# Performance work log

Measured on AMD Instinct MI355X. Metric: run time of the kernel, lower is better.

## Reference

```python
import jax, jax.numpy as jnp
import numpy as np

N, E, H, NF, EF = 50000, 400000, 128, 10, 10


def setup_inputs() -> dict:
    key = jax.random.key(0)
    ks = iter(jax.random.split(key, 24))
    rn = lambda shape, s=0.1: jax.random.normal(next(ks), shape, jnp.float32) * s
    z = lambda shape: jnp.zeros(shape, jnp.float32)
    o = lambda shape: jnp.ones(shape, jnp.float32)
    return {
        "x": jax.random.normal(next(ks), (N, NF), jnp.float32),
        "edge_index": jax.random.randint(next(ks), (2, E), 0, N, jnp.int32),
        "edge_attr": jax.random.normal(next(ks), (E, EF), jnp.float32),
        "ne_w": rn((NF, H)), "ne_b": z(H), "ne_g": o(H), "ne_beta": z(H),
        "ee_w": rn((EF, H)), "ee_b": z(H), "ee_g": o(H), "ee_beta": z(H),
        "gate_w": rn((3 * H, H)), "gate_b": z(H),
        "gatA_w": rn((2, H, H)), "gatA_asrc": rn((2, 8, 16)), "gatA_adst": rn((2, 8, 16)), "gatA_bias": z((2, H)),
        "gatB_w": rn((H, H)), "gatB_asrc": rn((1, H)), "gatB_adst": rn((1, H)), "gatB_bias": z(H),
        "ln_g": o((3, H)), "ln_b": z((3, H)),
        "c1_w": rn((2 * H, H)), "c1_b": z(H), "cl1_g": o(H), "cl1_b": z(H),
        "c2_w": rn((H, H // 2)), "c2_b": z(H // 2), "cl2_g": o(H // 2), "cl2_b": z(H // 2),
        "c3_w": rn((H // 2, 2)), "c3_b": z(2),
    }


def _ln(x, g, b):
    m = x.mean(-1, keepdims=True)
    v = ((x - m) ** 2).mean(-1, keepdims=True)
    return (x - m) / jnp.sqrt(v + 1e-5) * g + b


def _gat(h, src, dst, n, w, asrc, adst, bias, concat):
    # PyG GATConv: lin (no bias), per-edge leaky_relu score, segment softmax over dst, scatter-add
    heads, dout = asrc.shape
    xp = (h @ w).reshape(n, heads, dout)             # [N, heads, dout]
    a_s = (xp * asrc).sum(-1)                        # [N, heads]
    a_d = (xp * adst).sum(-1)
    e = jax.nn.leaky_relu(a_s[src] + a_d[dst], 0.2)  # [E2, heads]
    m = jax.ops.segment_max(e, dst, num_segments=n)
    ex = jnp.exp(e - m[dst])
    s = jax.ops.segment_sum(ex, dst, num_segments=n)
    alpha = ex / s[dst]                               # [E2, heads]
    out = jax.ops.segment_sum(xp[src] * alpha[..., None], dst, num_segments=n)  # [N, heads, dout]
    out = out.reshape(n, heads * dout) if concat else out.mean(1)
    return out + bias


def reference(x, edge_index, edge_attr, ne_w, ne_b, ne_g, ne_beta, ee_w, ee_b, ee_g, ee_beta,
              gate_w, gate_b, gatA_w, gatA_asrc, gatA_adst, gatA_bias, gatB_w, gatB_asrc,
              gatB_adst, gatB_bias, ln_g, ln_b, c1_w, c1_b, cl1_g, cl1_b, c2_w, c2_b,
              cl2_g, cl2_b, c3_w, c3_b):
    n = x.shape[0]
    row, col = edge_index[0], edge_index[1]
    loops = jnp.arange(n, dtype=edge_index.dtype)     # GATConv add_self_loops=True
    src_sl = jnp.concatenate([row, loops])
    dst_sl = jnp.concatenate([col, loops])

    h = jax.nn.relu(_ln(x @ ne_w + ne_b, ne_g, ne_beta))      # node encoder (dropout=eval)
    for l in range(2):
        h = _gat(h, src_sl, dst_sl, n, gatA_w[l], gatA_asrc[l], gatA_adst[l], gatA_bias[l], True)
        h = jax.nn.relu(_ln(h, ln_g[l], ln_b[l]))
    h = _gat(h, src_sl, dst_sl, n, gatB_w, gatB_asrc, gatB_adst, gatB_bias, False)
    h = jax.nn.relu(_ln(h, ln_g[2], ln_b[2]))

    s = h[row]
    d = h[col]
    e = jax.nn.relu(_ln(edge_attr @ ee_w + ee_b, ee_g, ee_beta))  # edge encoder
    gate = jax.nn.sigmoid(jnp.concatenate([s, d, e], axis=1) @ gate_w + gate_b)
    s = s + gate * e
    d = d + gate * e

    zc = jax.nn.relu(_ln(jnp.concatenate([s, d], axis=1) @ c1_w + c1_b, cl1_g, cl1_b))
    zc = jax.nn.relu(_ln(zc @ c2_w + c2_b, cl2_g, cl2_b))
    return zc @ c3_w + c3_b                                   # [E, num_classes]
```

## Files before the change

kernel.cpp:

```cpp
#include <hip/hip_runtime.h>
#include <hip/hip_bf16.h>

#define H 128
#define NFEAT 10
#define EFEAT 10
#define XPS 144

typedef __attribute__((ext_vector_type(8))) short bf16x8;
typedef __attribute__((ext_vector_type(4))) float f32x4;
typedef __attribute__((ext_vector_type(16))) float f32x16;
typedef __attribute__((ext_vector_type(4))) unsigned u32x4;
typedef __attribute__((ext_vector_type(2))) unsigned u32x2;

__device__ __forceinline__ float bflo(unsigned v) { return __uint_as_float(v << 16); }
__device__ __forceinline__ float bfhi(unsigned v) { return __uint_as_float(v & 0xffff0000u); }
__device__ __forceinline__ unsigned bfpack(float a, float b) {
    __hip_bfloat16 h0 = __float2bfloat16(a), h1 = __float2bfloat16(b);
    return (unsigned)(*(unsigned short*)&h0) | ((unsigned)(*(unsigned short*)&h1) << 16);
}
__device__ __forceinline__ bf16x8 cast8(u32x4 v) { return __builtin_bit_cast(bf16x8, v); }

__device__ __forceinline__ bf16x8 frag_from_pack(const unsigned* w, int b2) {
    u32x4 t;
    t.x = w[b2 * 4 + 0];
    t.y = w[b2 * 4 + 1];
    t.z = w[b2 * 4 + 2];
    t.w = w[b2 * 4 + 3];
    return cast8(t);
}

template<int NT>
__device__ __forceinline__ void bias_ln_relu_pack(f32x16* acc, const float* __restrict__ bias,
        const float* __restrict__ g, const float* __restrict__ beta,
        int hh, float invn, unsigned (*pk)[8]) {
    float sm = 0.f;
#pragma unroll
    for (int m = 0; m < NT; m++) {
#pragma unroll
        for (int P = 0; P < 4; P++) {
            f32x4 bv = *(const f32x4*)&bias[m * 32 + P * 8 + hh * 4];
#pragma unroll
            for (int u = 0; u < 4; u++) {
                float v = acc[m][P * 4 + u] + bv[u];
                acc[m][P * 4 + u] = v;
                sm += v;
            }
        }
    }
    sm += __shfl_xor(sm, 32, 64);
    float mean = sm * invn;
    float q = 0.f;
#pragma unroll
    for (int m = 0; m < NT; m++) {
#pragma unroll
        for (int r = 0; r < 16; r++) { float d = acc[m][r] - mean; q += d * d; }
    }
    q += __shfl_xor(q, 32, 64);
    float rstd = rsqrtf(q * invn + 1e-5f);
#pragma unroll
    for (int m = 0; m < NT; m++) {
#pragma unroll
        for (int P = 0; P < 4; P++) {
            f32x4 gv = *(const f32x4*)&g[m * 32 + P * 8 + hh * 4];
            f32x4 bz = *(const f32x4*)&beta[m * 32 + P * 8 + hh * 4];
#pragma unroll
            for (int u = 0; u < 4; u++) {
                float y = fmaxf((acc[m][P * 4 + u] - mean) * rstd * gv[u] + bz[u], 0.f);
                acc[m][P * 4 + u] = y;
            }
        }
    }
#pragma unroll
    for (int m = 0; m < NT; m++) {
#pragma unroll
        for (int p = 0; p < 8; p++) pk[m][p] = bfpack(acc[m][2 * p], acc[m][2 * p + 1]);
    }
}

__global__ __launch_bounds__(256) void k_degree(const int* __restrict__ col,
                                                int* __restrict__ deg, int E, int N) {
    int i = blockIdx.x * blockDim.x + threadIdx.x;
    int E2 = E + N;
    if (i < E2) {
        int d = (i < E) ? col[i] : (i - E);
        atomicAdd(&deg[d], 1);
    }
}

__global__ __launch_bounds__(1024) void k_scan(const int* __restrict__ deg,
                                               int* __restrict__ offs,
                                               int* __restrict__ cursor, int N) {
    __shared__ int ps[1024];
    int t = threadIdx.x;
    int chunk = (N + 1023) / 1024;
    int begin = t * chunk;
    int end = begin + chunk; if (end > N) end = N;
    int s = 0;
    for (int i = begin; i < end; i++) s += deg[i];
    if (begin >= N) s = 0;
    ps[t] = s;
    __syncthreads();
    for (int off = 1; off < 1024; off <<= 1) {
        int v = (t >= off) ? ps[t - off] : 0;
        __syncthreads();
        ps[t] += v;
        __syncthreads();
    }
    int run = (t == 0) ? 0 : ps[t - 1];
    if (begin < N) {
        for (int i = begin; i < end; i++) {
            offs[i] = run;
            cursor[i] = run;
            run += deg[i];
        }
    }
    if (t == 1023) offs[N] = ps[1023];
}

__global__ __launch_bounds__(256) void k_scatter(const int* __restrict__ rowp,
                                                 const int* __restrict__ colp,
                                                 int* __restrict__ cursor,
                                                 int* __restrict__ srcs, int E, int N) {
    int i = blockIdx.x * blockDim.x + threadIdx.x;
    if (i < E + N) {
        int s, d;
        if (i < E) { s = rowp[i]; d = colp[i]; }
        else       { s = i - E;  d = i - E; }
        int pos = atomicAdd(&cursor[d], 1);
        srcs[pos] = s;
    }
}

__global__ __launch_bounds__(256) void k_node_enc(const float* __restrict__ x,
                                                  const float* __restrict__ wm,
                                                  const float* __restrict__ b,
                                                  const float* __restrict__ g,
                                                  const float* __restrict__ beta,
                                                  __hip_bfloat16* __restrict__ h, int N) {
    int t = threadIdx.x;
    int w = t >> 6, l = t & 63;
    int n = blockIdx.x * 4 + w;
    if (n >= N) return;
    float xs[NFEAT];
#pragma unroll
    for (int k = 0; k < NFEAT; k++) xs[k] = x[(size_t)n * NFEAT + k];
    float a0 = b[2 * l], a1 = b[2 * l + 1];
#pragma unroll
    for (int k = 0; k < NFEAT; k++) {
        float2 wv = *(const float2*)&wm[k * H + 2 * l];
        a0 += xs[k] * wv.x;
        a1 += xs[k] * wv.y;
    }
    float p = a0 + a1;
#pragma unroll
    for (int s = 1; s < 64; s <<= 1) p += __shfl_xor(p, s, 64);
    float mean = p * (1.0f / H);
    float d0 = a0 - mean, d1 = a1 - mean;
    float q = d0 * d0 + d1 * d1;
#pragma unroll
    for (int s = 1; s < 64; s <<= 1) q += __shfl_xor(q, s, 64);
    float rstd = rsqrtf(q * (1.0f / H) + 1e-5f);
    float y0 = fmaxf(d0 * rstd * g[2 * l] + beta[2 * l], 0.0f);
    float y1 = fmaxf(d1 * rstd * g[2 * l + 1] + beta[2 * l + 1], 0.0f);
    *(unsigned*)&h[(size_t)n * H + 2 * l] = bfpack(y0, y1);
}

__global__ __launch_bounds__(256, 2) void k_gat_xp_mfma(
        const __hip_bfloat16* __restrict__ h_bf,
        const __hip_bfloat16* __restrict__ wT,
        const float* __restrict__ asrc,
        const float* __restrict__ adst,
        __hip_bfloat16* __restrict__ xp_bf,
        float* __restrict__ a_d,
        int heads, int N) {
    __shared__ __hip_bfloat16 Ws[128 * 136];
    __shared__ __hip_bfloat16 As[64 * 136];
    int t = threadIdx.x;
    int n0 = blockIdx.x * 64;

#pragma unroll
    for (int it = 0; it < 2; it++) {
        int idx = it * 256 + t;
        int row = idx >> 2, seg = idx & 3;
        const uint4* src = (const uint4*)(wT + row * 128 + seg * 32);
        uint4 v0 = src[0], v1 = src[1], v2 = src[2], v3 = src[3];
        uint4* dst = (uint4*)&Ws[row * 136 + seg * 32];
        dst[0] = v0; dst[1] = v1; dst[2] = v2; dst[3] = v3;
    }
    {
        int row = t >> 2, seg = t & 3;
        int n = n0 + row; if (n >= N) n = N - 1;
        const uint4* src = (const uint4*)(h_bf + (size_t)n * 128 + seg * 32);
        uint4 v0 = src[0], v1 = src[1], v2 = src[2], v3 = src[3];
        uint4* dst = (uint4*)&As[row * 136 + seg * 32];
        dst[0] = v0; dst[1] = v1; dst[2] = v2; dst[3] = v3;
    }
    __syncthreads();

    int w = t >> 6, l = t & 63, ln15 = l & 15, quad = l >> 4, q8 = quad * 8;
    f32x4 acc[8] = {};
#pragma unroll
    for (int k = 0; k < 128; k += 32) {
        bf16x8 af = *(const bf16x8*)&As[(w * 16 + ln15) * 136 + k + q8];
#pragma unroll
        for (int i = 0; i < 8; i++) {
            bf16x8 bfr = *(const bf16x8*)&Ws[(i * 16 + ln15) * 136 + k + q8];
            acc[i] = __builtin_amdgcn_mfma_f32_16x16x32_bf16(af, bfr, acc[i], 0, 0, 0);
        }
    }

    if (heads == 8) {
#pragma unroll
        for (int i = 0; i < 8; i++) {
            float av = asrc[i * 16 + ln15], dvv = adst[i * 16 + ln15];
            float ps[4], pd[4];
#pragma unroll
            for (int r = 0; r < 4; r++) { ps[r] = acc[i][r] * av; pd[r] = acc[i][r] * dvv; }
#pragma unroll
            for (int s = 1; s < 16; s <<= 1) {
#pragma unroll
                for (int r = 0; r < 4; r++) {
                    ps[r] += __shfl_xor(ps[r], s, 64);
                    pd[r] += __shfl_xor(pd[r], s, 64);
                }
            }
            if (ln15 == 0) {
#pragma unroll
                for (int r = 0; r < 4; r++) {
                    int n = n0 + w * 16 + quad * 4 + r;
                    if (n < N) {
                        *(float*)&xp_bf[(size_t)n * XPS + 128 + 2 * i] = ps[r];
                        a_d[(size_t)n * 8 + i] = pd[r];
                    }
                }
            }
        }
    } else {
        float ps[4] = {0, 0, 0, 0}, pd[4] = {0, 0, 0, 0};
#pragma unroll
        for (int i = 0; i < 8; i++) {
            float av = asrc[i * 16 + ln15], dvv = adst[i * 16 + ln15];
#pragma unroll
            for (int r = 0; r < 4; r++) { ps[r] += acc[i][r] * av; pd[r] += acc[i][r] * dvv; }
        }
#pragma unroll
        for (int s = 1; s < 16; s <<= 1) {
#pragma unroll
            for (int r = 0; r < 4; r++) {
                ps[r] += __shfl_xor(ps[r], s, 64);
                pd[r] += __shfl_xor(pd[r], s, 64);
            }
        }
        if (ln15 == 0) {
#pragma unroll
            for (int r = 0; r < 4; r++) {
                int n = n0 + w * 16 + quad * 4 + r;
                if (n < N) {
                    *(float*)&xp_bf[(size_t)n * XPS + 128] = ps[r];
                    a_d[n] = pd[r];
                }
            }
        }
    }

#pragma unroll
    for (int i = 0; i < 8; i++) {
#pragma unroll
        for (int r = 0; r < 4; r++) {
            int n = n0 + w * 16 + quad * 4 + r;
            if (n < N) xp_bf[(size_t)n * XPS + i * 16 + ln15] = __float2bfloat16(acc[i][r]);
        }
    }
}

__global__ __launch_bounds__(256) void k_gat_agg(const __hip_bfloat16* __restrict__ xp,
                                                 const float* __restrict__ a_d,
                                                 const int* __restrict__ offs,
                                                 const int* __restrict__ srcs,
                                                 const float* __restrict__ bias,
                                                 const float* __restrict__ g,
                                                 const float* __restrict__ b,
                                                 __hip_bfloat16* __restrict__ hout,
                                                 int heads, int N) {
    int t = threadIdx.x;
    int w = t >> 6, l = t & 63;
    int n = blockIdx.x * 4 + w;
    if (n >= N) return;
    int head = (heads == 8) ? (l >> 3) : 0;
    float adv = a_d[(size_t)n * heads + head];
    int s0 = offs[n], s1 = offs[n + 1];
    float acc0 = 0.0f, acc1 = 0.0f, den = 0.0f;
    int j = s0;
    for (; j + 4 <= s1; j += 4) {
        int s_[4];
#pragma unroll
        for (int u = 0; u < 4; u++) s_[u] = srcs[j + u];
        float e_[4]; unsigned v_[4];
#pragma unroll
        for (int u = 0; u < 4; u++) {
            const __hip_bfloat16* xr = xp + (size_t)s_[u] * XPS;
            e_[u] = ((const float*)xr)[64 + head];
            v_[u] = *(const unsigned*)&xr[2 * l];
        }
#pragma unroll
        for (int u = 0; u < 4; u++) {
            float e = e_[u] + adv;
            e = (e >= 0.0f) ? e : 0.2f * e;
            float ex = __expf(e);
            den += ex;
            acc0 += ex * bflo(v_[u]);
            acc1 += ex * bfhi(v_[u]);
        }
    }
    for (; j < s1; j++) {
        int s = srcs[j];
        const __hip_bfloat16* xr = xp + (size_t)s * XPS;
        float e = ((const float*)xr)[64 + head] + adv;
        e = (e >= 0.0f) ? e : 0.2f * e;
        float ex = __expf(e);
        den += ex;
        unsigned v = *(const unsigned*)&xr[2 * l];
        acc0 += ex * bflo(v);
        acc1 += ex * bfhi(v);
    }
    float inv = 1.0f / den;
    float v0 = acc0 * inv + bias[2 * l];
    float v1 = acc1 * inv + bias[2 * l + 1];
    float p = v0 + v1;
#pragma unroll
    for (int s = 1; s < 64; s <<= 1) p += __shfl_xor(p, s, 64);
    float mean = p * (1.0f / H);
    float d0 = v0 - mean, d1 = v1 - mean;
    float q = d0 * d0 + d1 * d1;
#pragma unroll
    for (int s = 1; s < 64; s <<= 1) q += __shfl_xor(q, s, 64);
    float rstd = rsqrtf(q * (1.0f / H) + 1e-5f);
    float y0 = fmaxf(d0 * rstd * g[2 * l] + b[2 * l], 0.0f);
    float y1 = fmaxf(d1 * rstd * g[2 * l + 1] + b[2 * l + 1], 0.0f);
    *(unsigned*)&hout[(size_t)n * H + 2 * l] = bfpack(y0, y1);
}

__global__ __launch_bounds__(256) void k_wprep(const float* __restrict__ gate_w,
                                               const float* __restrict__ c1_w,
                                               const float* __restrict__ c2_w,
                                               const float* __restrict__ gatA_w,
                                               const float* __restrict__ gatB_w,
                                               const float* __restrict__ ee_w,
                                               __hip_bfloat16* __restrict__ gate_sw,
                                               __hip_bfloat16* __restrict__ c1_sw,
                                               __hip_bfloat16* __restrict__ c2_sw,
                                               __hip_bfloat16* __restrict__ wT3,
                                               __hip_bfloat16* __restrict__ ee_sw) {
    int i = blockIdx.x * blockDim.x + threadIdx.x;
    if (i < 49152) {
        int j = i & 7, l = (i >> 3) & 63, s = i >> 9;
        int m = s & 3, ks = s >> 2;
        int hh = l >> 5;
        int k;
        if (ks < 8) k = 256 + ks * 16 + 4 * hh + (j & 3) + 8 * (j >> 2);
        else        k = (ks - 8) * 16 + hh * 8 + j;
        int n = m * 32 + (l & 31);
        gate_sw[i] = __float2bfloat16(gate_w[k * 128 + n]);
    } else if (i < 81920) {
        int mm = i - 49152;
        int j = mm & 7, l = (mm >> 3) & 63, s = mm >> 9;
        int m = s & 3, ks = s >> 2;
        int k = ks * 16 + 4 * (l >> 5) + (j & 3) + 8 * (j >> 2);
        int n = m * 32 + (l & 31);
        c1_sw[mm] = __float2bfloat16(c1_w[k * 128 + n]);
    } else if (i < 90112) {
        int mm = i - 81920;
        int j = mm & 7, l = (mm >> 3) & 63, s = mm >> 9;
        int m = s & 1, ks = s >> 1;
        int k = ks * 16 + 4 * (l >> 5) + (j & 3) + 8 * (j >> 2);
        int n = m * 32 + (l & 31);
        c2_sw[mm] = __float2bfloat16(c2_w[k * 64 + n]);
    } else if (i < 139264) {
        int m = i - 90112;
        int mat = m / 16384, r = m % 16384;
        int n = r / 128, k = r % 128;
        const float* src = (mat < 2) ? (gatA_w + (size_t)mat * 16384) : gatB_w;
        wT3[m] = __float2bfloat16(src[k * 128 + n]);
    } else if (i < 141312) {
        int mm = i - 139264;
        int j = mm & 7, l = (mm >> 3) & 63, s = mm >> 9;
        int k = (l >> 5) * 8 + j;
        int n = s * 32 + (l & 31);
        ee_sw[mm] = (k < EFEAT) ? __float2bfloat16(ee_w[k * 128 + n]) : __float2bfloat16(0.0f);
    }
}

__global__ __launch_bounds__(256, 2) void k_edge_cls_mfma32(
        const __hip_bfloat16* __restrict__ h_bf,
        const int* __restrict__ rowp, const int* __restrict__ colp,
        const float* __restrict__ eattr,
        const __hip_bfloat16* __restrict__ ee_fa, const float* __restrict__ ee_b,
        const float* __restrict__ ee_g, const float* __restrict__ ee_beta,
        const __hip_bfloat16* __restrict__ gate_fa, const float* __restrict__ gate_b,
        const __hip_bfloat16* __restrict__ c1_fa, const float* __restrict__ c1_b,
        const float* __restrict__ cl1_g, const float* __restrict__ cl1_b,
        const __hip_bfloat16* __restrict__ c2_fa, const float* __restrict__ c2_b,
        const float* __restrict__ cl2_g, const float* __restrict__ cl2_b,
        const float* __restrict__ c3_w, const float* __restrict__ c3_b,
        float* __restrict__ out, int E) {
    int t = threadIdx.x;
    int w = t >> 6, l = t & 63;
    int hh = l >> 5, e32 = l & 31;
    int eIdx = blockIdx.x * 128 + w * 32 + e32;
    int eF = (eIdx < E) ? eIdx : (E - 1);
    int ri = rowp[eF], ci = colp[eF];
    const unsigned short* rS = (const unsigned short*)h_bf + (size_t)ri * H;
    const unsigned short* rD = (const unsigned short*)h_bf + (size_t)ci * H;

    unsigned efw[4][8];
    {
        const char* eb = (const char*)(eattr + (size_t)eF * EFEAT);
        float2 p0 = *(const float2*)(eb + (hh << 5));
        float2 p1 = *(const float2*)(eb + 8);
        float2 p2 = *(const float2*)(eb + 16);
        float2 p3 = *(const float2*)(eb + 24);
        if (hh) { p1.x = p1.y = 0.f; p2.x = p2.y = 0.f; p3.x = p3.y = 0.f; }
        u32x4 bwv;
        bwv.x = bfpack(p0.x, p0.y);
        bwv.y = bfpack(p1.x, p1.y);
        bwv.z = bfpack(p2.x, p2.y);
        bwv.w = bfpack(p3.x, p3.y);
        bf16x8 bb = cast8(bwv);
        f32x16 acc[4] = {};
#pragma unroll
        for (int m = 0; m < 4; m++) {
            bf16x8 a = *(const bf16x8*)(ee_fa + ((size_t)m * 64 + l) * 8);
            acc[m] = __builtin_amdgcn_mfma_f32_32x32x16_bf16(a, bb, acc[m], 0, 0, 0);
        }
        bias_ln_relu_pack<4>(acc, ee_b, ee_g, ee_beta, hh, 1.f / 128.f, efw);
    }

    f32x16 acc1[4] = {};
    {
        bf16x8 af[4];
#pragma unroll
        for (int s = 0; s < 4; s++) af[s] = *(const bf16x8*)(gate_fa + ((size_t)s * 64 + l) * 8);
#pragma unroll
        for (int ks = 0; ks < 8; ks++) {
            int m = ks >> 1, b2 = ks & 1;
            bf16x8 bb = frag_from_pack(efw[m], b2);
#pragma unroll
            for (int mt = 0; mt < 4; mt++) {
                int s = ks * 4 + mt;
                bf16x8 a = af[s & 3];
                af[s & 3] = *(const bf16x8*)(gate_fa + ((size_t)(s + 4) * 64 + l) * 8);
                acc1[mt] = __builtin_amdgcn_mfma_f32_32x32x16_bf16(a, bb, acc1[mt], 0, 0, 0);
            }
        }
#pragma unroll
        for (int ks = 8; ks < 24; ks++) {
            const unsigned short* rp = (ks < 16) ? rS : rD;
            int kl = ((ks - 8) & 7) * 16 + hh * 8;
            bf16x8 bb = *(const bf16x8*)(rp + kl);
#pragma unroll
            for (int mt = 0; mt < 4; mt++) {
                int s = ks * 4 + mt;
                bf16x8 a = af[s & 3];
                if (s + 4 < 96) af[s & 3] = *(const bf16x8*)(gate_fa + ((size_t)(s + 4) * 64 + l) * 8);
                acc1[mt] = __builtin_amdgcn_mfma_f32_32x32x16_bf16(a, bb, acc1[mt], 0, 0, 0);
            }
        }
    }

    unsigned sw[4][8], dw[4][8];
    {
#pragma unroll
        for (int m = 0; m < 4; m++) {
#pragma unroll
            for (int P = 0; P < 4; P++) {
                int f0 = m * 32 + P * 8 + hh * 4;
                f32x4 gb = *(const f32x4*)&gate_b[f0];
                u32x2 sv = *(const u32x2*)(rS + f0);
                u32x2 dv = *(const u32x2*)(rD + f0);
#pragma unroll
                for (int u2 = 0; u2 < 2; u2++) {
                    int p = P * 2 + u2;
                    unsigned svw = u2 ? sv.y : sv.x;
                    unsigned dvw = u2 ? dv.y : dv.x;
                    float g0 = acc1[m][2 * p] + gb[2 * u2];
                    float g1 = acc1[m][2 * p + 1] + gb[2 * u2 + 1];
                    g0 = 1.f / (1.f + __expf(-g0));
                    g1 = 1.f / (1.f + __expf(-g1));
                    float e0 = bflo(efw[m][p]), e1 = bfhi(efw[m][p]);
                    sw[m][p] = bfpack(bflo(svw) + g0 * e0, bfhi(svw) + g1 * e1);
                    dw[m][p] = bfpack(bflo(dvw) + g0 * e0, bfhi(dvw) + g1 * e1);
                }
            }
        }
    }

    unsigned z1w[4][8];
    {
        f32x16 acc2[4] = {};
        bf16x8 af[4];
#pragma unroll
        for (int s = 0; s < 4; s++) af[s] = *(const bf16x8*)(c1_fa + ((size_t)s * 64 + l) * 8);
#pragma unroll
        for (int ks = 0; ks < 8; ks++) {
            int m = ks >> 1, b2 = ks & 1;
            bf16x8 bb = frag_from_pack(sw[m], b2);
#pragma unroll
            for (int mt = 0; mt < 4; mt++) {
                int s = ks * 4 + mt;
                bf16x8 a = af[s & 3];
                af[s & 3] = *(const bf16x8*)(c1_fa + ((size_t)(s + 4) * 64 + l) * 8);
                acc2[mt] = __builtin_amdgcn_mfma_f32_32x32x16_bf16(a, bb, acc2[mt], 0, 0, 0);
            }
        }
#pragma unroll
        for (int ks = 8; ks < 16; ks++) {
            int kk = ks - 8;
            int m = kk >> 1, b2 = kk & 1;
            bf16x8 bb = frag_from_pack(dw[m], b2);
#pragma unroll
            for (int mt = 0; mt < 4; mt++) {
                int s = ks * 4 + mt;
                bf16x8 a = af[s & 3];
                if (s + 4 < 64) af[s & 3] = *(const bf16x8*)(c1_fa + ((size_t)(s + 4) * 64 + l) * 8);
                acc2[mt] = __builtin_amdgcn_mfma_f32_32x32x16_bf16(a, bb, acc2[mt], 0, 0, 0);
            }
        }
        bias_ln_relu_pack<4>(acc2, c1_b, cl1_g, cl1_b, hh, 1.f / 128.f, z1w);
    }

    {
        f32x16 acc3[2] = {};
        bf16x8 af[4];
#pragma unroll
        for (int s = 0; s < 4; s++) af[s] = *(const bf16x8*)(c2_fa + ((size_t)s * 64 + l) * 8);
#pragma unroll
        for (int ks = 0; ks < 8; ks++) {
            int m = ks >> 1, b2 = ks & 1;
            bf16x8 bb = frag_from_pack(z1w[m], b2);
#pragma unroll
            for (int mt = 0; mt < 2; mt++) {
                int s = ks * 2 + mt;
                bf16x8 a = af[s & 3];
                if (s + 4 < 16) af[s & 3] = *(const bf16x8*)(c2_fa + ((size_t)(s + 4) * 64 + l) * 8);
                acc3[mt] = __builtin_amdgcn_mfma_f32_32x32x16_bf16(a, bb, acc3[mt], 0, 0, 0);
            }
        }
        float sm = 0.f;
#pragma unroll
        for (int m = 0; m < 2; m++) {
#pragma unroll
            for (int P = 0; P < 4; P++) {
                f32x4 bv = *(const f32x4*)&c2_b[m * 32 + P * 8 + hh * 4];
#pragma unroll
                for (int u = 0; u < 4; u++) {
                    float v = acc3[m][P * 4 + u] + bv[u];
                    acc3[m][P * 4 + u] = v;
                    sm += v;
                }
            }
        }
        sm += __shfl_xor(sm, 32, 64);
        float mean = sm * (1.f / 64.f);
        float q = 0.f;
#pragma unroll
        for (int m = 0; m < 2; m++) {
#pragma unroll
            for (int r = 0; r < 16; r++) { float d = acc3[m][r] - mean; q += d * d; }
        }
        q += __shfl_xor(q, 32, 64);
        float rstd = rsqrtf(q * (1.f / 64.f) + 1e-5f);
        float s0 = 0.f, s1 = 0.f;
#pragma unroll
        for (int m = 0; m < 2; m++) {
#pragma unroll
            for (int P = 0; P < 4; P++) {
                int f0 = m * 32 + P * 8 + hh * 4;
                f32x4 gv = *(const f32x4*)&cl2_g[f0];
                f32x4 bz = *(const f32x4*)&cl2_b[f0];
                f32x4 wA = *(const f32x4*)&c3_w[f0 * 2];
                f32x4 wB = *(const f32x4*)&c3_w[f0 * 2 + 4];
#pragma unroll
                for (int u = 0; u < 4; u++) {
                    float y = fmaxf((acc3[m][P * 4 + u] - mean) * rstd * gv[u] + bz[u], 0.f);
                    float wc0 = (u < 2) ? wA[2 * u] : wB[2 * u - 4];
                    float wc1 = (u < 2) ? wA[2 * u + 1] : wB[2 * u - 3];
                    s0 += y * wc0;
                    s1 += y * wc1;
                }
            }
        }
        s0 += __shfl_xor(s0, 32, 64);
        s1 += __shfl_xor(s1, 32, 64);
        if (hh == 0 && eIdx < E) {
            float2 o; o.x = s0 + c3_b[0]; o.y = s1 + c3_b[1];
            *(float2*)&out[(size_t)eIdx * 2] = o;
        }
    }
}

extern "C" void kernel_launch(void* const* d_in, const int* in_sizes, int n_in,
                              void* d_out, int out_size, void* d_ws, size_t ws_size,
                              hipStream_t stream) {
    const float* x        = (const float*)d_in[0];
    const int*   eidx     = (const int*)d_in[1];
    const float* eattr    = (const float*)d_in[2];
    const float* ne_w     = (const float*)d_in[3];
    const float* ne_b     = (const float*)d_in[4];
    const float* ne_g     = (const float*)d_in[5];
    const float* ne_beta  = (const float*)d_in[6];
    const float* ee_w     = (const float*)d_in[7];
    const float* ee_b     = (const float*)d_in[8];
    const float* ee_g     = (const float*)d_in[9];
    const float* ee_beta  = (const float*)d_in[10];
    const float* gate_w   = (const float*)d_in[11];
    const float* gate_b   = (const float*)d_in[12];
    const float* gatA_w   = (const float*)d_in[13];
    const float* gatA_as  = (const float*)d_in[14];
    const float* gatA_ad  = (const float*)d_in[15];
    const float* gatA_bias= (const float*)d_in[16];
    const float* gatB_w   = (const float*)d_in[17];
    const float* gatB_as  = (const float*)d_in[18];
    const float* gatB_ad  = (const float*)d_in[19];
    const float* gatB_bias= (const float*)d_in[20];
    const float* ln_g     = (const float*)d_in[21];
    const float* ln_b     = (const float*)d_in[22];
    const float* c1_w     = (const float*)d_in[23];
    const float* c1_b     = (const float*)d_in[24];
    const float* cl1_g    = (const float*)d_in[25];
    const float* cl1_b    = (const float*)d_in[26];
    const float* c2_w     = (const float*)d_in[27];
    const float* c2_b     = (const float*)d_in[28];
    const float* cl2_g    = (const float*)d_in[29];
    const float* cl2_b    = (const float*)d_in[30];
    const float* c3_w     = (const float*)d_in[31];
    const float* c3_b     = (const float*)d_in[32];

    const int N = in_sizes[0] / NFEAT;
    const int E = in_sizes[1] / 2;
    const int E2 = E + N;
    const int* rowp = eidx;
    const int* colp = eidx + E;

    char* ws = (char*)d_ws;
    size_t off = 0;
    auto alloc = [&](size_t bytes) -> void* {
        void* p = ws + off;
        off = (off + bytes + 255) & ~(size_t)255;
        return p;
    };
    int*   deg    = (int*)alloc((size_t)N * 4);
    int*   cursor = (int*)alloc((size_t)N * 4);
    int*   offs   = (int*)alloc((size_t)(N + 1) * 4);
    int*   srcs   = (int*)alloc((size_t)E2 * 4);
    float* a_d    = (float*)alloc((size_t)N * 8 * 4);
    __hip_bfloat16* h_bfA  = (__hip_bfloat16*)alloc((size_t)N * H * 2);
    __hip_bfloat16* h_bfB  = (__hip_bfloat16*)alloc((size_t)N * H * 2);
    __hip_bfloat16* xp_bf  = (__hip_bfloat16*)alloc((size_t)N * XPS * 2);
    __hip_bfloat16* gate_sw= (__hip_bfloat16*)alloc((size_t)49152 * 2);
    __hip_bfloat16* c1_sw  = (__hip_bfloat16*)alloc((size_t)32768 * 2);
    __hip_bfloat16* c2_sw  = (__hip_bfloat16*)alloc((size_t)8192 * 2);
    __hip_bfloat16* wT3    = (__hip_bfloat16*)alloc((size_t)3 * 128 * 128 * 2);
    __hip_bfloat16* ee_sw  = (__hip_bfloat16*)alloc((size_t)4096 * 2);
    (void)ws_size;

    k_wprep<<<(141312 + 255) / 256, 256, 0, stream>>>(gate_w, c1_w, c2_w, gatA_w, gatB_w, ee_w,
                                                      gate_sw, c1_sw, c2_sw, wT3, ee_sw);

    hipMemsetAsync(deg, 0, (size_t)N * 4, stream);
    k_degree<<<(E2 + 255) / 256, 256, 0, stream>>>(colp, deg, E, N);
    k_scan<<<1, 1024, 0, stream>>>(deg, offs, cursor, N);
    k_scatter<<<(E2 + 255) / 256, 256, 0, stream>>>(rowp, colp, cursor, srcs, E, N);

    int ngrid = (N + 3) / 4;
    k_node_enc<<<ngrid, 256, 0, stream>>>(x, ne_w, ne_b, ne_g, ne_beta, h_bfA, N);

    int xpgrid = (N + 63) / 64;
    __hip_bfloat16* hin = h_bfA;
    __hip_bfloat16* hout = h_bfB;
    for (int l = 0; l < 2; l++) {
        k_gat_xp_mfma<<<xpgrid, 256, 0, stream>>>(hin, wT3 + (size_t)l * 16384,
                                                  gatA_as + l * H, gatA_ad + l * H,
                                                  xp_bf, a_d, 8, N);
        k_gat_agg<<<ngrid, 256, 0, stream>>>(xp_bf, a_d, offs, srcs,
                                             gatA_bias + l * H, ln_g + l * H, ln_b + l * H,
                                             hout, 8, N);
        __hip_bfloat16* tmp = hin; hin = hout; hout = tmp;
    }
    k_gat_xp_mfma<<<xpgrid, 256, 0, stream>>>(hin, wT3 + (size_t)2 * 16384,
                                              gatB_as, gatB_ad,
                                              xp_bf, a_d, 1, N);
    k_gat_agg<<<ngrid, 256, 0, stream>>>(xp_bf, a_d, offs, srcs,
                                         gatB_bias, ln_g + 2 * H, ln_b + 2 * H,
                                         hout, 1, N);

    k_edge_cls_mfma32<<<(E + 127) / 128, 256, 0, stream>>>(
        hout, rowp, colp, eattr,
        ee_sw, ee_b, ee_g, ee_beta,
        gate_sw, gate_b,
        c1_sw, c1_b, cl1_g, cl1_b,
        c2_sw, c2_b, cl2_g, cl2_b,
        c3_w, c3_b,
        (float*)d_out, E);
}
```

Before: 675.5 us.

## Precompute per-node gate and classifier projections, gather them per edge

Exploits linearity: the gate and first classifier layers applied to h[row] and h[col] are computed once per node (N×4 GEMMs into an fp32 table) instead of once per edge. The edge kernel then gathers these projections and only multiplies the gated edge-encoder term, using c1 weights summed over the src and dst halves. This cuts per-edge MFMA work from 24+16 K-steps to 8+8. In exchange it adds a 100MB fp32 table whose random gathers of 2KB rows per edge may become memory-bound.

After: 718.4 us. 6.4% more time.

```diff
diff --git a/kernel.cpp b/kernel.cpp
--- a/kernel.cpp
+++ b/kernel.cpp
@@ -346,58 +346,116 @@
                                                const float* __restrict__ gatA_w,
                                                const float* __restrict__ gatB_w,
                                                const float* __restrict__ ee_w,
-                                               __hip_bfloat16* __restrict__ gate_sw,
-                                               __hip_bfloat16* __restrict__ c1_sw,
+                                               __hip_bfloat16* __restrict__ gef_sw,
+                                               __hip_bfloat16* __restrict__ c1s_sw,
                                                __hip_bfloat16* __restrict__ c2_sw,
+                                               __hip_bfloat16* __restrict__ ee_sw,
                                                __hip_bfloat16* __restrict__ wT3,
-                                               __hip_bfloat16* __restrict__ ee_sw) {
+                                               __hip_bfloat16* __restrict__ wpre4) {
     int i = blockIdx.x * blockDim.x + threadIdx.x;
-    if (i < 49152) {
+    if (i < 16384) {
         int j = i & 7, l = (i >> 3) & 63, s = i >> 9;
         int m = s & 3, ks = s >> 2;
-        int hh = l >> 5;
-        int k;
-        if (ks < 8) k = 256 + ks * 16 + 4 * hh + (j & 3) + 8 * (j >> 2);
-        else        k = (ks - 8) * 16 + hh * 8 + j;
+        int k = 256 + ks * 16 + 4 * (l >> 5) + (j & 3) + 8 * (j >> 2);
         int n = m * 32 + (l & 31);
-        gate_sw[i] = __float2bfloat16(gate_w[k * 128 + n]);
-    } else if (i < 81920) {
-        int mm = i - 49152;
+        gef_sw[i] = __float2bfloat16(gate_w[k * 128 + n]);
+    } else if (i < 32768) {
+        int mm = i - 16384;
         int j = mm & 7, l = (mm >> 3) & 63, s = mm >> 9;
         int m = s & 3, ks = s >> 2;
         int k = ks * 16 + 4 * (l >> 5) + (j & 3) + 8 * (j >> 2);
         int n = m * 32 + (l & 31);
-        c1_sw[mm] = __float2bfloat16(c1_w[k * 128 + n]);
-    } else if (i < 90112) {
-        int mm = i - 81920;
+        c1s_sw[mm] = __float2bfloat16(c1_w[k * 128 + n] + c1_w[(128 + k) * 128 + n]);
+    } else if (i < 40960) {
+        int mm = i - 32768;
         int j = mm & 7, l = (mm >> 3) & 63, s = mm >> 9;
         int m = s & 1, ks = s >> 1;
         int k = ks * 16 + 4 * (l >> 5) + (j & 3) + 8 * (j >> 2);
         int n = m * 32 + (l & 31);
         c2_sw[mm] = __float2bfloat16(c2_w[k * 64 + n]);
-    } else if (i < 139264) {
-        int m = i - 90112;
-        int mat = m / 16384, r = m % 16384;
-        int n = r / 128, k = r % 128;
-        const float* src = (mat < 2) ? (gatA_w + (size_t)mat * 16384) : gatB_w;
-        wT3[m] = __float2bfloat16(src[k * 128 + n]);
-    } else if (i < 141312) {
-        int mm = i - 139264;
+    } else if (i < 43008) {
+        int mm = i - 40960;
         int j = mm & 7, l = (mm >> 3) & 63, s = mm >> 9;
         int k = (l >> 5) * 8 + j;
         int n = s * 32 + (l & 31);
         ee_sw[mm] = (k < EFEAT) ? __float2bfloat16(ee_w[k * 128 + n]) : __float2bfloat16(0.0f);
-    }
-}
-
-__global__ __launch_bounds__(256, 2) void k_edge_cls_mfma32(
+    } else if (i < 92160) {
+        int mm = i - 43008;
+        int mat = mm / 16384, r = mm % 16384;
+        int n = r / 128, k = r % 128;
+        const float* src = (mat < 2) ? (gatA_w + (size_t)mat * 16384) : gatB_w;
+        wT3[mm] = __float2bfloat16(src[k * 128 + n]);
+    } else if (i < 157696) {
+        int mm = i - 92160;
+        int mat = mm / 16384, r = mm % 16384;
+        int n = r / 128, k = r % 128;
+        float v = (mat == 0) ? gate_w[k * 128 + n]
+                : (mat == 1) ? gate_w[(128 + k) * 128 + n]
+                : (mat == 2) ? c1_w[k * 128 + n]
+                             : c1_w[(128 + k) * 128 + n];
+        wpre4[mm] = __float2bfloat16(v);
+    }
+}
+
+__global__ __launch_bounds__(256, 2) void k_pre_gemm(
         const __hip_bfloat16* __restrict__ h_bf,
+        const __hip_bfloat16* __restrict__ wpre4,
+        float* __restrict__ pre, int N) {
+    __shared__ __hip_bfloat16 Ws[128 * 136];
+    __shared__ __hip_bfloat16 As[64 * 136];
+    int t = threadIdx.x;
+    int n0 = blockIdx.x * 64;
+    int mat = blockIdx.y;
+    const __hip_bfloat16* wT = wpre4 + (size_t)mat * 16384;
+
+#pragma unroll
+    for (int it = 0; it < 2; it++) {
+        int idx = it * 256 + t;
+        int row = idx >> 2, seg = idx & 3;
+        const uint4* src = (const uint4*)(wT + row * 128 + seg * 32);
+        uint4 v0 = src[0], v1 = src[1], v2 = src[2], v3 = src[3];
+        uint4* dst = (uint4*)&Ws[row * 136 + seg * 32];
+        dst[0] = v0; dst[1] = v1; dst[2] = v2; dst[3] = v3;
+    }
+    {
+        int row = t >> 2, seg = t & 3;
+        int n = n0 + row; if (n >= N) n = N - 1;
+        const uint4* src = (const uint4*)(h_bf + (size_t)n * 128 + seg * 32);
+        uint4 v0 = src[0], v1 = src[1], v2 = src[2], v3 = src[3];
+        uint4* dst = (uint4*)&As[row * 136 + seg * 32];
+        dst[0] = v0; dst[1] = v1; dst[2] = v2; dst[3] = v3;
+    }
+    __syncthreads();
+
+    int w = t >> 6, l = t & 63, ln15 = l & 15, quad = l >> 4, q8 = quad * 8;
+    f32x4 acc[8] = {};
+#pragma unroll
+    for (int k = 0; k < 128; k += 32) {
+        bf16x8 af = *(const bf16x8*)&As[(w * 16 + ln15) * 136 + k + q8];
+#pragma unroll
+        for (int i = 0; i < 8; i++) {
+            bf16x8 bfr = *(const bf16x8*)&Ws[(i * 16 + ln15) * 136 + k + q8];
+            acc[i] = __builtin_amdgcn_mfma_f32_16x16x32_bf16(af, bfr, acc[i], 0, 0, 0);
+        }
+    }
+#pragma unroll
+    for (int i = 0; i < 8; i++) {
+#pragma unroll
+        for (int r = 0; r < 4; r++) {
+            int n = n0 + w * 16 + quad * 4 + r;
+            if (n < N) pre[(size_t)n * 512 + mat * 128 + i * 16 + ln15] = acc[i][r];
+        }
+    }
+}
+
+__global__ __launch_bounds__(256, 3) void k_edge_cls_v5(
         const int* __restrict__ rowp, const int* __restrict__ colp,
         const float* __restrict__ eattr,
+        const float* __restrict__ pre,
         const __hip_bfloat16* __restrict__ ee_fa, const float* __restrict__ ee_b,
         const float* __restrict__ ee_g, const float* __restrict__ ee_beta,
-        const __hip_bfloat16* __restrict__ gate_fa, const float* __restrict__ gate_b,
-        const __hip_bfloat16* __restrict__ c1_fa, const float* __restrict__ c1_b,
+        const __hip_bfloat16* __restrict__ gef_fa, const float* __restrict__ gate_b,
+        const __hip_bfloat16* __restrict__ c1s_fa, const float* __restrict__ c1_b,
         const float* __restrict__ cl1_g, const float* __restrict__ cl1_b,
         const __hip_bfloat16* __restrict__ c2_fa, const float* __restrict__ c2_b,
         const float* __restrict__ cl2_g, const float* __restrict__ cl2_b,
@@ -408,9 +466,8 @@
     int hh = l >> 5, e32 = l & 31;
     int eIdx = blockIdx.x * 128 + w * 32 + e32;
     int eF = (eIdx < E) ? eIdx : (E - 1);
-    int ri = rowp[eF], ci = colp[eF];
-    const unsigned short* rS = (const unsigned short*)h_bf + (size_t)ri * H;
-    const unsigned short* rD = (const unsigned short*)h_bf + (size_t)ci * H;
+    const float* pS = pre + (size_t)rowp[eF] * 512;
+    const float* pD = pre + (size_t)colp[eF] * 512;
 
     unsigned efw[4][8];
     {
@@ -439,35 +496,21 @@
     {
         bf16x8 af[4];
 #pragma unroll
-        for (int s = 0; s < 4; s++) af[s] = *(const bf16x8*)(gate_fa + ((size_t)s * 64 + l) * 8);
+        for (int s = 0; s < 4; s++) af[s] = *(const bf16x8*)(gef_fa + ((size_t)s * 64 + l) * 8);
 #pragma unroll
         for (int ks = 0; ks < 8; ks++) {
-            int m = ks >> 1, b2 = ks & 1;
-            bf16x8 bb = frag_from_pack(efw[m], b2);
+            bf16x8 bb = frag_from_pack(efw[ks >> 1], ks & 1);
 #pragma unroll
             for (int mt = 0; mt < 4; mt++) {
                 int s = ks * 4 + mt;
                 bf16x8 a = af[s & 3];
-                af[s & 3] = *(const bf16x8*)(gate_fa + ((size_t)(s + 4) * 64 + l) * 8);
+                if (s + 4 < 32) af[s & 3] = *(const bf16x8*)(gef_fa + ((size_t)(s + 4) * 64 + l) * 8);
                 acc1[mt] = __builtin_amdgcn_mfma_f32_32x32x16_bf16(a, bb, acc1[mt], 0, 0, 0);
             }
         }
-#pragma unroll
-        for (int ks = 8; ks < 24; ks++) {
-            const unsigned short* rp = (ks < 16) ? rS : rD;
-            int kl = ((ks - 8) & 7) * 16 + hh * 8;
-            bf16x8 bb = *(const bf16x8*)(rp + kl);
-#pragma unroll
-            for (int mt = 0; mt < 4; mt++) {
-                int s = ks * 4 + mt;
-                bf16x8 a = af[s & 3];
-                if (s + 4 < 96) af[s & 3] = *(const bf16x8*)(gate_fa + ((size_t)(s + 4) * 64 + l) * 8);
-                acc1[mt] = __builtin_amdgcn_mfma_f32_32x32x16_bf16(a, bb, acc1[mt], 0, 0, 0);
-            }
-        }
-    }
-
-    unsigned sw[4][8], dw[4][8];
+    }
+
+    unsigned gew[4][8];
     {
 #pragma unroll
         for (int m = 0; m < 4; m++) {
@@ -475,20 +518,16 @@
             for (int P = 0; P < 4; P++) {
                 int f0 = m * 32 + P * 8 + hh * 4;
                 f32x4 gb = *(const f32x4*)&gate_b[f0];
-                u32x2 sv = *(const u32x2*)(rS + f0);
-                u32x2 dv = *(const u32x2*)(rD + f0);
+                f32x4 uu = *(const f32x4*)(pS + f0);
+                f32x4 vv = *(const f32x4*)(pD + 128 + f0);
 #pragma unroll
                 for (int u2 = 0; u2 < 2; u2++) {
                     int p = P * 2 + u2;
-                    unsigned svw = u2 ? sv.y : sv.x;
-                    unsigned dvw = u2 ? dv.y : dv.x;
-                    float g0 = acc1[m][2 * p] + gb[2 * u2];
-                    float g1 = acc1[m][2 * p + 1] + gb[2 * u2 + 1];
+                    float g0 = acc1[m][2 * p]     + uu[2 * u2]     + vv[2 * u2]     + gb[2 * u2];
+                    float g1 = acc1[m][2 * p + 1] + uu[2 * u2 + 1] + vv[2 * u2 + 1] + gb[2 * u2 + 1];
                     g0 = 1.f / (1.f + __expf(-g0));
                     g1 = 1.f / (1.f + __expf(-g1));
-                    float e0 = bflo(efw[m][p]), e1 = bfhi(efw[m][p]);
-                    sw[m][p] = bfpack(bflo(svw) + g0 * e0, bfhi(svw) + g1 * e1);
-                    dw[m][p] = bfpack(bflo(dvw) + g0 * e0, bfhi(dvw) + g1 * e1);
+                    gew[m][p] = bfpack(g0 * bflo(efw[m][p]), g1 * bfhi(efw[m][p]));
                 }
             }
         }
@@ -499,30 +538,27 @@
         f32x16 acc2[4] = {};
         bf16x8 af[4];
 #pragma unroll
-        for (int s = 0; s < 4; s++) af[s] = *(const bf16x8*)(c1_fa + ((size_t)s * 64 + l) * 8);
+        for (int s = 0; s < 4; s++) af[s] = *(const bf16x8*)(c1s_fa + ((size_t)s * 64 + l) * 8);
 #pragma unroll
         for (int ks = 0; ks < 8; ks++) {
-            int m = ks >> 1, b2 = ks & 1;
-            bf16x8 bb = frag_from_pack(sw[m], b2);
+            bf16x8 bb = frag_from_pack(gew[ks >> 1], ks & 1);
 #pragma unroll
             for (int mt = 0; mt < 4; mt++) {
                 int s = ks * 4 + mt;
                 bf16x8 a = af[s & 3];
-                af[s & 3] = *(const bf16x8*)(c1_fa + ((size_t)(s + 4) * 64 + l) * 8);
+                if (s + 4 < 32) af[s & 3] = *(const bf16x8*)(c1s_fa + ((size_t)(s + 4) * 64 + l) * 8);
                 acc2[mt] = __builtin_amdgcn_mfma_f32_32x32x16_bf16(a, bb, acc2[mt], 0, 0, 0);
             }
         }
 #pragma unroll
-        for (int ks = 8; ks < 16; ks++) {
-            int kk = ks - 8;
-            int m = kk >> 1, b2 = kk & 1;
-            bf16x8 bb = frag_from_pack(dw[m], b2);
-#pragma unroll
-            for (int mt = 0; mt < 4; mt++) {
-                int s = ks * 4 + mt;
-                bf16x8 a = af[s & 3];
-                if (s + 4 < 64) af[s & 3] = *(const bf16x8*)(c1_fa + ((size_t)(s + 4) * 64 + l) * 8);
-                acc2[mt] = __builtin_amdgcn_mfma_f32_32x32x16_bf16(a, bb, acc2[mt], 0, 0, 0);
+        for (int m = 0; m < 4; m++) {
+#pragma unroll
+            for (int P = 0; P < 4; P++) {
+                int f0 = m * 32 + P * 8 + hh * 4;
+                f32x4 pp = *(const f32x4*)(pS + 256 + f0);
+                f32x4 qq = *(const f32x4*)(pD + 384 + f0);
+#pragma unroll
+                for (int u = 0; u < 4; u++) acc2[m][P * 4 + u] += pp[u] + qq[u];
             }
         }
         bias_ln_relu_pack<4>(acc2, c1_b, cl1_g, cl1_b, hh, 1.f / 128.f, z1w);
@@ -535,8 +571,7 @@
         for (int s = 0; s < 4; s++) af[s] = *(const bf16x8*)(c2_fa + ((size_t)s * 64 + l) * 8);
 #pragma unroll
         for (int ks = 0; ks < 8; ks++) {
-            int m = ks >> 1, b2 = ks & 1;
-            bf16x8 bb = frag_from_pack(z1w[m], b2);
+            bf16x8 bb = frag_from_pack(z1w[ks >> 1], ks & 1);
 #pragma unroll
             for (int mt = 0; mt < 2; mt++) {
                 int s = ks * 2 + mt;
@@ -656,15 +691,17 @@
     __hip_bfloat16* h_bfA  = (__hip_bfloat16*)alloc((size_t)N * H * 2);
     __hip_bfloat16* h_bfB  = (__hip_bfloat16*)alloc((size_t)N * H * 2);
     __hip_bfloat16* xp_bf  = (__hip_bfloat16*)alloc((size_t)N * XPS * 2);
-    __hip_bfloat16* gate_sw= (__hip_bfloat16*)alloc((size_t)49152 * 2);
-    __hip_bfloat16* c1_sw  = (__hip_bfloat16*)alloc((size_t)32768 * 2);
+    __hip_bfloat16* gef_sw = (__hip_bfloat16*)alloc((size_t)16384 * 2);
+    __hip_bfloat16* c1s_sw = (__hip_bfloat16*)alloc((size_t)16384 * 2);
     __hip_bfloat16* c2_sw  = (__hip_bfloat16*)alloc((size_t)8192 * 2);
+    __hip_bfloat16* ee_sw  = (__hip_bfloat16*)alloc((size_t)2048 * 2);
     __hip_bfloat16* wT3    = (__hip_bfloat16*)alloc((size_t)3 * 128 * 128 * 2);
-    __hip_bfloat16* ee_sw  = (__hip_bfloat16*)alloc((size_t)4096 * 2);
+    __hip_bfloat16* wpre4  = (__hip_bfloat16*)alloc((size_t)4 * 128 * 128 * 2);
+    float*          pre    = (float*)alloc((size_t)N * 512 * 4);
     (void)ws_size;
 
-    k_wprep<<<(141312 + 255) / 256, 256, 0, stream>>>(gate_w, c1_w, c2_w, gatA_w, gatB_w, ee_w,
-                                                      gate_sw, c1_sw, c2_sw, wT3, ee_sw);
+    k_wprep<<<(157696 + 255) / 256, 256, 0, stream>>>(gate_w, c1_w, c2_w, gatA_w, gatB_w, ee_w,
+                                                      gef_sw, c1s_sw, c2_sw, ee_sw, wT3, wpre4);
 
     hipMemsetAsync(deg, 0, (size_t)N * 4, stream);
     k_degree<<<(E2 + 255) / 256, 256, 0, stream>>>(colp, deg, E, N);
@@ -693,11 +730,14 @@
                                          gatB_bias, ln_g + 2 * H, ln_b + 2 * H,
                                          hout, 1, N);
 
-    k_edge_cls_mfma32<<<(E + 127) / 128, 256, 0, stream>>>(
-        hout, rowp, colp, eattr,
+    dim3 gpre(xpgrid, 4);
+    k_pre_gemm<<<gpre, 256, 0, stream>>>(hout, wpre4, pre, N);
+
+    k_edge_cls_v5<<<(E + 127) / 128, 256, 0, stream>>>(
+        rowp, colp, eattr, pre,
         ee_sw, ee_b, ee_g, ee_beta,
-        gate_sw, gate_b,
-        c1_sw, c1_b, cl1_g, cl1_b,
+        gef_sw, gate_b,
+        c1s_sw, c1_b, cl1_g, cl1_b,
         c2_sw, c2_b, cl2_g, cl2_b,
         c3_w, c3_b,
         (float*)d_out, E);
```

## Stage edge-classifier intermediates in LDS and deepen GAT aggregation unroll

Applied to the files above, without the earlier changes.

The edge classifier kernel now keeps the encoded edge features, gated src/dst vectors and the c1 output in a per-edge shared-memory row instead of packed register arrays. The weight-prep permutation is changed so B fragments can be read directly from that row. The MFMA loops drop manual A-fragment prefetching and are rolled with unroll 1, cutting register pressure at the cost of LDS traffic and less load/compute overlap. Separately, GAT aggregation gains an 8-wide unrolled edge loop to put more gathers in flight.

Result: slower. 721.9 us (+6.9%).

```diff
diff --git a/kernel.cpp b/kernel.cpp
--- a/kernel.cpp
+++ b/kernel.cpp
@@ -5,6 +5,7 @@
 #define NFEAT 10
 #define EFEAT 10
 #define XPS 144
+#define BROW2 264
 
 typedef __attribute__((ext_vector_type(8))) short bf16x8;
 typedef __attribute__((ext_vector_type(4))) float f32x4;
@@ -20,19 +21,10 @@
 }
 __device__ __forceinline__ bf16x8 cast8(u32x4 v) { return __builtin_bit_cast(bf16x8, v); }
 
-__device__ __forceinline__ bf16x8 frag_from_pack(const unsigned* w, int b2) {
-    u32x4 t;
-    t.x = w[b2 * 4 + 0];
-    t.y = w[b2 * 4 + 1];
-    t.z = w[b2 * 4 + 2];
-    t.w = w[b2 * 4 + 3];
-    return cast8(t);
-}
-
 template<int NT>
-__device__ __forceinline__ void bias_ln_relu_pack(f32x16* acc, const float* __restrict__ bias,
+__device__ __forceinline__ void bias_ln_relu_st(f32x16* acc, const float* __restrict__ bias,
         const float* __restrict__ g, const float* __restrict__ beta,
-        int hh, float invn, unsigned (*pk)[8]) {
+        int hh, float invn, __hip_bfloat16* Brow) {
     float sm = 0.f;
 #pragma unroll
     for (int m = 0; m < NT; m++) {
@@ -73,7 +65,10 @@
 #pragma unroll
     for (int m = 0; m < NT; m++) {
 #pragma unroll
-        for (int p = 0; p < 8; p++) pk[m][p] = bfpack(acc[m][2 * p], acc[m][2 * p + 1]);
+        for (int p = 0; p < 8; p++) {
+            int feat = 32 * m + 8 * (p >> 1) + 4 * hh + 2 * (p & 1);
+            *(unsigned*)&Brow[feat] = bfpack(acc[m][2 * p], acc[m][2 * p + 1]);
+        }
     }
 }
 
@@ -291,6 +286,27 @@
     int s0 = offs[n], s1 = offs[n + 1];
     float acc0 = 0.0f, acc1 = 0.0f, den = 0.0f;
     int j = s0;
+    for (; j + 8 <= s1; j += 8) {
+        int s_[8];
+#pragma unroll
+        for (int u = 0; u < 8; u++) s_[u] = srcs[j + u];
+        float e_[8]; unsigned v_[8];
+#pragma unroll
+        for (int u = 0; u < 8; u++) {
+            const __hip_bfloat16* xr = xp + (size_t)s_[u] * XPS;
+            e_[u] = ((const float*)xr)[64 + head];
+            v_[u] = *(const unsigned*)&xr[2 * l];
+        }
+#pragma unroll
+        for (int u = 0; u < 8; u++) {
+            float e = e_[u] + adv;
+            e = (e >= 0.0f) ? e : 0.2f * e;
+            float ex = __expf(e);
+            den += ex;
+            acc0 += ex * bflo(v_[u]);
+            acc1 += ex * bfhi(v_[u]);
+        }
+    }
     for (; j + 4 <= s1; j += 4) {
         int s_[4];
 #pragma unroll
@@ -356,23 +372,22 @@
         int j = i & 7, l = (i >> 3) & 63, s = i >> 9;
         int m = s & 3, ks = s >> 2;
         int hh = l >> 5;
-        int k;
-        if (ks < 8) k = 256 + ks * 16 + 4 * hh + (j & 3) + 8 * (j >> 2);
-        else        k = (ks - 8) * 16 + hh * 8 + j;
+        int k = (ks < 8) ? (256 + ks * 16 + hh * 8 + j)
+                         : ((ks - 8) * 16 + hh * 8 + j);
         int n = m * 32 + (l & 31);
         gate_sw[i] = __float2bfloat16(gate_w[k * 128 + n]);
     } else if (i < 81920) {
         int mm = i - 49152;
         int j = mm & 7, l = (mm >> 3) & 63, s = mm >> 9;
         int m = s & 3, ks = s >> 2;
-        int k = ks * 16 + 4 * (l >> 5) + (j & 3) + 8 * (j >> 2);
+        int k = ks * 16 + (l >> 5) * 8 + j;
         int n = m * 32 + (l & 31);
         c1_sw[mm] = __float2bfloat16(c1_w[k * 128 + n]);
     } else if (i < 90112) {
         int mm = i - 81920;
         int j = mm & 7, l = (mm >> 3) & 63, s = mm >> 9;
         int m = s & 1, ks = s >> 1;
-        int k = ks * 16 + 4 * (l >> 5) + (j & 3) + 8 * (j >> 2);
+        int k = ks * 16 + (l >> 5) * 8 + j;
         int n = m * 32 + (l & 31);
         c2_sw[mm] = __float2bfloat16(c2_w[k * 64 + n]);
     } else if (i < 139264) {
@@ -390,7 +405,7 @@
     }
 }
 
-__global__ __launch_bounds__(256, 2) void k_edge_cls_mfma32(
+__global__ __launch_bounds__(256, 2) void k_edge_cls_v9(
         const __hip_bfloat16* __restrict__ h_bf,
         const int* __restrict__ rowp, const int* __restrict__ colp,
         const float* __restrict__ eattr,
@@ -403,16 +418,16 @@
         const float* __restrict__ cl2_g, const float* __restrict__ cl2_b,
         const float* __restrict__ c3_w, const float* __restrict__ c3_b,
         float* __restrict__ out, int E) {
+    __shared__ __hip_bfloat16 Bs[4 * 32 * BROW2];
     int t = threadIdx.x;
     int w = t >> 6, l = t & 63;
     int hh = l >> 5, e32 = l & 31;
+    __hip_bfloat16* Brow = Bs + ((size_t)(w * 32 + e32)) * BROW2;
     int eIdx = blockIdx.x * 128 + w * 32 + e32;
     int eF = (eIdx < E) ? eIdx : (E - 1);
-    int ri = rowp[eF], ci = colp[eF];
-    const unsigned short* rS = (const unsigned short*)h_bf + (size_t)ri * H;
-    const unsigned short* rD = (const unsigned short*)h_bf + (size_t)ci * H;
-
-    unsigned efw[4][8];
+    const unsigned short* rS = (const unsigned short*)h_bf + (size_t)rowp[eF] * H;
+    const unsigned short* rD = (const unsigned short*)h_bf + (size_t)colp[eF] * H;
+
     {
         const char* eb = (const char*)(eattr + (size_t)eF * EFEAT);
         float2 p0 = *(const float2*)(eb + (hh << 5));
@@ -432,42 +447,38 @@
             bf16x8 a = *(const bf16x8*)(ee_fa + ((size_t)m * 64 + l) * 8);
             acc[m] = __builtin_amdgcn_mfma_f32_32x32x16_bf16(a, bb, acc[m], 0, 0, 0);
         }
-        bias_ln_relu_pack<4>(acc, ee_b, ee_g, ee_beta, hh, 1.f / 128.f, efw);
+        bias_ln_relu_st<4>(acc, ee_b, ee_g, ee_beta, hh, 1.f / 128.f, Brow);
     }
 
     f32x16 acc1[4] = {};
     {
-        bf16x8 af[4];
-#pragma unroll
-        for (int s = 0; s < 4; s++) af[s] = *(const bf16x8*)(gate_fa + ((size_t)s * 64 + l) * 8);
-#pragma unroll
+        const bf16x8* wp = (const bf16x8*)gate_fa + l;
+#pragma unroll 1
         for (int ks = 0; ks < 8; ks++) {
-            int m = ks >> 1, b2 = ks & 1;
-            bf16x8 bb = frag_from_pack(efw[m], b2);
-#pragma unroll
-            for (int mt = 0; mt < 4; mt++) {
-                int s = ks * 4 + mt;
-                bf16x8 a = af[s & 3];
-                af[s & 3] = *(const bf16x8*)(gate_fa + ((size_t)(s + 4) * 64 + l) * 8);
-                acc1[mt] = __builtin_amdgcn_mfma_f32_32x32x16_bf16(a, bb, acc1[mt], 0, 0, 0);
-            }
-        }
-#pragma unroll
-        for (int ks = 8; ks < 24; ks++) {
-            const unsigned short* rp = (ks < 16) ? rS : rD;
-            int kl = ((ks - 8) & 7) * 16 + hh * 8;
-            bf16x8 bb = *(const bf16x8*)(rp + kl);
-#pragma unroll
-            for (int mt = 0; mt < 4; mt++) {
-                int s = ks * 4 + mt;
-                bf16x8 a = af[s & 3];
-                if (s + 4 < 96) af[s & 3] = *(const bf16x8*)(gate_fa + ((size_t)(s + 4) * 64 + l) * 8);
-                acc1[mt] = __builtin_amdgcn_mfma_f32_32x32x16_bf16(a, bb, acc1[mt], 0, 0, 0);
-            }
-        }
-    }
-
-    unsigned sw[4][8], dw[4][8];
+            bf16x8 bb = *(const bf16x8*)&Brow[ks * 16 + hh * 8];
+#pragma unroll
+            for (int mt = 0; mt < 4; mt++)
+                acc1[mt] = __builtin_amdgcn_mfma_f32_32x32x16_bf16(
+                    wp[(size_t)(ks * 4 + mt) * 64], bb, acc1[mt], 0, 0, 0);
+        }
+#pragma unroll 1
+        for (int ks = 8; ks < 16; ks++) {
+            bf16x8 bb = *(const bf16x8*)(rS + (ks - 8) * 16 + hh * 8);
+#pragma unroll
+            for (int mt = 0; mt < 4; mt++)
+                acc1[mt] = __builtin_amdgcn_mfma_f32_32x32x16_bf16(
+                    wp[(size_t)(ks * 4 + mt) * 64], bb, acc1[mt], 0, 0, 0);
+        }
+#pragma unroll 1
+        for (int ks = 16; ks < 24; ks++) {
+            bf16x8 bb = *(const bf16x8*)(rD + (ks - 16) * 16 + hh * 8);
+#pragma unroll
+            for (int mt = 0; mt < 4; mt++)
+                acc1[mt] = __builtin_amdgcn_mfma_f32_32x32x16_bf16(
+                    wp[(size_t)(ks * 4 + mt) * 64], bb, acc1[mt], 0, 0, 0);
+        }
+    }
+
     {
 #pragma unroll
         for (int m = 0; m < 4; m++) {
@@ -480,70 +491,46 @@
 #pragma unroll
                 for (int u2 = 0; u2 < 2; u2++) {
                     int p = P * 2 + u2;
+                    int feat = f0 + 2 * u2;
                     unsigned svw = u2 ? sv.y : sv.x;
                     unsigned dvw = u2 ? dv.y : dv.x;
                     float g0 = acc1[m][2 * p] + gb[2 * u2];
                     float g1 = acc1[m][2 * p + 1] + gb[2 * u2 + 1];
                     g0 = 1.f / (1.f + __expf(-g0));
                     g1 = 1.f / (1.f + __expf(-g1));
-                    float e0 = bflo(efw[m][p]), e1 = bfhi(efw[m][p]);
-                    sw[m][p] = bfpack(bflo(svw) + g0 * e0, bfhi(svw) + g1 * e1);
-                    dw[m][p] = bfpack(bflo(dvw) + g0 * e0, bfhi(dvw) + g1 * e1);
+                    unsigned ew = *(unsigned*)&Brow[feat];
+                    float e0 = bflo(ew), e1 = bfhi(ew);
+                    *(unsigned*)&Brow[feat]       = bfpack(bflo(svw) + g0 * e0, bfhi(svw) + g1 * e1);
+                    *(unsigned*)&Brow[128 + feat] = bfpack(bflo(dvw) + g0 * e0, bfhi(dvw) + g1 * e1);
                 }
             }
         }
     }
 
-    unsigned z1w[4][8];
     {
         f32x16 acc2[4] = {};
-        bf16x8 af[4];
-#pragma unroll
-        for (int s = 0; s < 4; s++) af[s] = *(const bf16x8*)(c1_fa + ((size_t)s * 64 + l) * 8);
-#pragma unroll
-        for (int ks = 0; ks < 8; ks++) {
-            int m = ks >> 1, b2 = ks & 1;
-            bf16x8 bb = frag_from_pack(sw[m], b2);
-#pragma unroll
-            for (int mt = 0; mt < 4; mt++) {
-                int s = ks * 4 + mt;
-                bf16x8 a = af[s & 3];
-                af[s & 3] = *(const bf16x8*)(c1_fa + ((size_t)(s + 4) * 64 + l) * 8);
-                acc2[mt] = __builtin_amdgcn_mfma_f32_32x32x16_bf16(a, bb, acc2[mt], 0, 0, 0);
-            }
-        }
-#pragma unroll
-        for (int ks = 8; ks < 16; ks++) {
-            int kk = ks - 8;
-            int m = kk >> 1, b2 = kk & 1;
-            bf16x8 bb = frag_from_pack(dw[m], b2);
-#pragma unroll
-            for (int mt = 0; mt < 4; mt++) {
-                int s = ks * 4 + mt;
-                bf16x8 a = af[s & 3];
-                if (s + 4 < 64) af[s & 3] = *(const bf16x8*)(c1_fa + ((size_t)(s + 4) * 64 + l) * 8);
-                acc2[mt] = __builtin_amdgcn_mfma_f32_32x32x16_bf16(a, bb, acc2[mt], 0, 0, 0);
-            }
-        }
-        bias_ln_relu_pack<4>(acc2, c1_b, cl1_g, cl1_b, hh, 1.f / 128.f, z1w);
+        const bf16x8* wp = (const bf16x8*)c1_fa + l;
+#pragma unroll 1
+        for (int ks = 0; ks < 16; ks++) {
+            bf16x8 bb = *(const bf16x8*)&Brow[ks * 16 + hh * 8];
+#pragma unroll
+            for (int mt = 0; mt < 4; mt++)
+                acc2[mt] = __builtin_amdgcn_mfma_f32_32x32x16_bf16(
+                    wp[(size_t)(ks * 4 + mt) * 64], bb, acc2[mt], 0, 0, 0);
+        }
+        bias_ln_relu_st<4>(acc2, c1_b, cl1_g, cl1_b, hh, 1.f / 128.f, Brow);
     }
 
     {
         f32x16 acc3[2] = {};
-        bf16x8 af[4];
-#pragma unroll
-        for (int s = 0; s < 4; s++) af[s] = *(const bf16x8*)(c2_fa + ((size_t)s * 64 + l) * 8);
-#pragma unroll
+        const bf16x8* wp = (const bf16x8*)c2_fa + l;
+#pragma unroll 1
         for (int ks = 0; ks < 8; ks++) {
-            int m = ks >> 1, b2 = ks & 1;
-            bf16x8 bb = frag_from_pack(z1w[m], b2);
-#pragma unroll
-            for (int mt = 0; mt < 2; mt++) {
-                int s = ks * 2 + mt;
-                bf16x8 a = af[s & 3];
-                if (s + 4 < 16) af[s & 3] = *(const bf16x8*)(c2_fa + ((size_t)(s + 4) * 64 + l) * 8);
-                acc3[mt] = __builtin_amdgcn_mfma_f32_32x32x16_bf16(a, bb, acc3[mt], 0, 0, 0);
-            }
+            bf16x8 bb = *(const bf16x8*)&Brow[ks * 16 + hh * 8];
+#pragma unroll
+            for (int mt = 0; mt < 2; mt++)
+                acc3[mt] = __builtin_amdgcn_mfma_f32_32x32x16_bf16(
+                    wp[(size_t)(ks * 2 + mt) * 64], bb, acc3[mt], 0, 0, 0);
         }
         float sm = 0.f;
 #pragma unroll
@@ -693,7 +680,7 @@
                                          gatB_bias, ln_g + 2 * H, ln_b + 2 * H,
                                          hout, 1, N);
 
-    k_edge_cls_mfma32<<<(E + 127) / 128, 256, 0, stream>>>(
+    k_edge_cls_v9<<<(E + 127) / 128, 256, 0, stream>>>(
         hout, rowp, colp, eattr,
         ee_sw, ee_b, ee_g, ee_beta,
         gate_sw, gate_b,
```
